# Performance work log

Measured on AMD Instinct MI355X. Metric: run time of the kernel, lower is better.

Reference implementation:

```python
import jax, jax.numpy as jnp
import numpy as np

U, I, D, NNZ, LAYERS, B = 50000, 50000, 64, 3200000, 3, 4096
N = U + I
L2_REG = 1e-5
EPS = 1e-12


def setup_inputs() -> dict:
    key = jax.random.key(0)
    ks = jax.random.split(key, 12)
    return {
        "users": jax.random.randint(ks[0], (B,), 0, U, dtype=jnp.int64)
        if jax.config.jax_enable_x64 else jax.random.randint(ks[0], (B,), 0, U, dtype=jnp.int32),
        "pos_items": jax.random.randint(ks[1], (B,), 0, N, dtype=jnp.int32),
        "neg_items": jax.random.randint(ks[2], (B,), 0, N, dtype=jnp.int32),
        "rows": jax.random.randint(ks[3], (NNZ,), 0, N, dtype=jnp.int32),
        "cols": jax.random.randint(ks[4], (NNZ,), 0, N, dtype=jnp.int32),
        "vals": jax.random.uniform(ks[5], (NNZ,), dtype=jnp.float32),
        "user_embed": jax.random.normal(ks[6], (U, D), dtype=jnp.float32),
        "item_embed": jax.random.normal(ks[7], (I, D), dtype=jnp.float32),
        "W1": jax.random.normal(ks[8], (LAYERS, D, D), dtype=jnp.float32) * 0.1,
        "b1": jax.random.normal(ks[9], (LAYERS, 1, D), dtype=jnp.float32) * 0.1,
        "W2": jax.random.normal(ks[10], (LAYERS, D, D), dtype=jnp.float32) * 0.1,
        "b2": jax.random.normal(ks[11], (LAYERS, 1, D), dtype=jnp.float32) * 0.1,
    }


def reference(users, pos_items, neg_items, rows, cols, vals,
              user_embed, item_embed, W1, b1, W2, b2):
    # E: [N, D] concatenated user/item embeddings
    E = jnp.concatenate([user_embed, item_embed], axis=0)
    embs = [E]
    for l in range(W1.shape[0]):
        # SpMM: L @ E via edge-wise gather + scatter-add (memory-bound)
        msgs = vals[:, None] * E[cols]                     # [nnz, D]
        L_mul = jax.ops.segment_sum(msgs, rows, num_segments=N)
        A_mul = L_mul + E                                  # A = L + I
        left = A_mul @ W1[l] + b1[l]
        right = (L_mul * E) @ W2[l] + b2[l]
        E = jax.nn.leaky_relu(left + right, negative_slope=0.2)
        # message dropout rate = 0 -> identity
        norm = jnp.maximum(jnp.linalg.norm(E, axis=1, keepdims=True), EPS)
        embs.append(E / norm)
    all_e = jnp.concatenate(embs, axis=1)                  # [N, D*(LAYERS+1)]
    u = all_e[users]
    p = all_e[pos_items]
    n = all_e[neg_items]
    pos_rating = jnp.sum(u * p, axis=1)
    neg_rating = jnp.sum(u * n, axis=1)
    bpr_loss = -jnp.mean(jax.nn.log_sigmoid(pos_rating - neg_rating))
    # faithful to source: neg term is ||n|| (not squared)
    l2norm = (jnp.sum(u ** 2) + jnp.sum(p ** 2) + jnp.sqrt(jnp.sum(n ** 2))) / 2.0
    l2reg = L2_REG * l2norm / u.shape[0]
    return bpr_loss + l2reg
```

## Files before the change

kernel.cpp:

```cpp
#include <hip/hip_runtime.h>
#include <hip/hip_bf16.h>
#include <math.h>

#define U_CNT 50000
#define I_CNT 50000
#define N_CNT 100000
#define D 64
#define NNZ_CNT 3200000
#define LAYERS 3
#define BATCH 4096
#define L2_REG_F 1e-5f
#define EPS_F 1e-12f

#define NBUCKET 391
#define SC_NBLK 256
#define SC_CHUNK 12500
#define BCNT_N (NBUCKET * SC_NBLK)
#define BCNT_NBLK ((BCNT_N + 255) / 256)

typedef __attribute__((ext_vector_type(8))) short short8;
typedef __attribute__((ext_vector_type(4))) float floatx4;

__device__ __forceinline__ unsigned short f32_to_bf16(float f) {
    unsigned int u = __float_as_uint(f);
    u += 0x7FFFu + ((u >> 16) & 1u);
    return (unsigned short)(u >> 16);
}
__device__ __forceinline__ float bf16_to_f32(unsigned short h) {
    return __uint_as_float(((unsigned int)h) << 16);
}
__device__ __forceinline__ float bf16_lo(unsigned int u) {
    return __uint_as_float(u << 16);
}
__device__ __forceinline__ float bf16_hi(unsigned int u) {
    return __uint_as_float(u & 0xFFFF0000u);
}
__device__ __forceinline__ unsigned int pack_bf16(float a, float b) {
    return (unsigned int)f32_to_bf16(a) | ((unsigned int)f32_to_bf16(b) << 16);
}

__global__ void init_E(const float* __restrict__ ue, const float* __restrict__ ie,
                       unsigned short* __restrict__ Ebf, float* __restrict__ all_e) {
    int tid = blockIdx.x * blockDim.x + threadIdx.x;
    if (tid >= N_CNT * D) return;
    int row = tid >> 6;
    int d = tid & 63;
    float v = (row < U_CNT) ? ue[tid] : ie[tid - U_CNT * D];
    Ebf[tid] = f32_to_bf16(v);
    all_e[(size_t)row * 256 + d] = v;
}

__global__ void scan_p1(const int* __restrict__ in, int* __restrict__ bsums, int n) {
    __shared__ int s[256];
    int t = threadIdx.x;
    int i = blockIdx.x * 256 + t;
    int v = (i < n) ? in[i] : 0;
    s[t] = v;
    __syncthreads();
    for (int off = 128; off >= 1; off >>= 1) {
        if (t < off) s[t] += s[t + off];
        __syncthreads();
    }
    if (t == 0) bsums[blockIdx.x] = s[0];
}

__global__ void scan_p2(int* __restrict__ bsums, int nblk) {
    __shared__ int s[512];
    int t = threadIdx.x;
    int v = (t < nblk) ? bsums[t] : 0;
    s[t] = v;
    __syncthreads();
    for (int off = 1; off < 512; off <<= 1) {
        int x = (t >= off) ? s[t - off] : 0;
        __syncthreads();
        s[t] += x;
        __syncthreads();
    }
    if (t < nblk) bsums[t] = s[t] - v;
}

__global__ void scan_p3(const int* __restrict__ in, const int* __restrict__ bsums,
                        int* __restrict__ out, int n) {
    __shared__ int s[256];
    int t = threadIdx.x;
    int i = blockIdx.x * 256 + t;
    int v = (i < n) ? in[i] : 0;
    s[t] = v;
    __syncthreads();
    for (int off = 1; off < 256; off <<= 1) {
        int x = (t >= off) ? s[t - off] : 0;
        __syncthreads();
        s[t] += x;
        __syncthreads();
    }
    if (i < n) out[i] = s[t] - v + bsums[blockIdx.x];
}

__global__ __launch_bounds__(1024) void bucket_hist(const int* __restrict__ rows,
                                                    int* __restrict__ bcnt) {
    __shared__ int h[NBUCKET];
    int blk = blockIdx.x, t = threadIdx.x;
    if (t < NBUCKET) h[t] = 0;
    __syncthreads();
    int s = blk * SC_CHUNK, e = s + SC_CHUNK;
    for (int i = s + t; i < e; i += 1024) atomicAdd(&h[rows[i] >> 8], 1);
    __syncthreads();
    if (t < NBUCKET) bcnt[t * SC_NBLK + blk] = h[t];
}

__global__ __launch_bounds__(1024) void block_scatter(const int* __restrict__ rows,
                                                      const int* __restrict__ cols,
                                                      const float* __restrict__ vals,
                                                      const int* __restrict__ boff,
                                                      float2* __restrict__ bbuf) {
    __shared__ int cur[NBUCKET];
    int blk = blockIdx.x, t = threadIdx.x;
    if (t < NBUCKET) cur[t] = boff[t * SC_NBLK + blk];
    __syncthreads();
    int s = blk * SC_CHUNK, e = s + SC_CHUNK;
    for (int i = s + t; i < e; i += 1024) {
        int r = rows[i];
        int b = r >> 8;
        int p = atomicAdd(&cur[b], 1);
        unsigned int bits = ((unsigned int)(r & 255) << 17) | (unsigned int)cols[i];
        bbuf[p] = make_float2(vals[i], __uint_as_float(bits));
    }
}

__global__ __launch_bounds__(1024) void csr_finalize(const float2* __restrict__ bbuf,
                                                     const int* __restrict__ boff,
                                                     int* __restrict__ row_ptr,
                                                     float2* __restrict__ packed) {
    __shared__ int h[256];
    __shared__ int cur[256];
    int b = blockIdx.x, t = threadIdx.x;
    int s = boff[b * SC_NBLK];
    int e = (b == NBUCKET - 1) ? NNZ_CNT : boff[(b + 1) * SC_NBLK];
    if (t < 256) h[t] = 0;
    __syncthreads();
    for (int i = s + t; i < e; i += 1024)
        atomicAdd(&h[__float_as_uint(bbuf[i].y) >> 17], 1);
    __syncthreads();
    int v = (t < 256) ? h[t] : 0;
    for (int off = 1; off < 256; off <<= 1) {
        int x = (t >= off && t < 256) ? h[t - off] : 0;
        __syncthreads();
        if (t < 256) h[t] += x;
        __syncthreads();
    }
    if (t < 256) {
        int start = s + h[t] - v;
        int row = (b << 8) + t;
        if (row < N_CNT) row_ptr[row] = start;
        cur[t] = start;
        if (b == 0 && t == 0) row_ptr[N_CNT] = NNZ_CNT;
    }
    __syncthreads();
    for (int i = s + t; i < e; i += 1024) {
        float2 rec = bbuf[i];
        unsigned int bits = __float_as_uint(rec.y);
        int p = atomicAdd(&cur[bits >> 17], 1);
        packed[p] = make_float2(rec.x, __int_as_float(bits & 0x1FFFFu));
    }
}

__global__ __launch_bounds__(256) void spmm_bf16(const float2* __restrict__ packed,
                                                 const int* __restrict__ row_ptr,
                                                 const unsigned short* __restrict__ Ebf,
                                                 unsigned short* __restrict__ Lm) {
    int wid = (blockIdx.x * blockDim.x + threadIdx.x) >> 6;
    int lane = threadIdx.x & 63;
    if (wid >= N_CNT) return;
    int s = row_ptr[wid];
    int e = row_ptr[wid + 1];
    int sub = lane >> 2;
    int sl = lane & 3;
    int eidx = sub >> 1;
    int half = sub & 1;
    int dbase = half * 32 + sl * 8;
    float a0 = 0.f, a1 = 0.f, a2 = 0.f, a3 = 0.f;
    float a4 = 0.f, a5 = 0.f, a6 = 0.f, a7 = 0.f;
    int i = s + eidx;
    float2 rec = (i < e) ? packed[i] : make_float2(0.f, __int_as_float(0));
    while (i < e) {
        int inext = i + 8;
        float2 rnext = (inext < e) ? packed[inext] : make_float2(0.f, __int_as_float(0));
        int c = __float_as_int(rec.y);
        uint4 ev = *(const uint4*)(Ebf + (size_t)c * D + dbase);
        float v = rec.x;
        a0 += v * bf16_lo(ev.x); a1 += v * bf16_hi(ev.x);
        a2 += v * bf16_lo(ev.y); a3 += v * bf16_hi(ev.y);
        a4 += v * bf16_lo(ev.z); a5 += v * bf16_hi(ev.z);
        a6 += v * bf16_lo(ev.w); a7 += v * bf16_hi(ev.w);
        rec = rnext;
        i = inext;
    }
#pragma unroll
    for (int off = 32; off >= 8; off >>= 1) {
        a0 += __shfl_xor(a0, off, 64); a1 += __shfl_xor(a1, off, 64);
        a2 += __shfl_xor(a2, off, 64); a3 += __shfl_xor(a3, off, 64);
        a4 += __shfl_xor(a4, off, 64); a5 += __shfl_xor(a5, off, 64);
        a6 += __shfl_xor(a6, off, 64); a7 += __shfl_xor(a7, off, 64);
    }
    if (eidx == 0) {
        unsigned int* dst = (unsigned int*)(Lm + (size_t)wid * D + dbase);
        *(uint4*)dst = make_uint4(pack_bf16(a0, a1), pack_bf16(a2, a3),
                                  pack_bf16(a4, a5), pack_bf16(a6, a7));
    }
}

#define AP 136
__global__ __launch_bounds__(256) void layer_fused_mfma(const unsigned short* __restrict__ Lm,
                                                        unsigned short* __restrict__ Ebf,
                                                        const float* __restrict__ W1,
                                                        const float* __restrict__ b1,
                                                        const float* __restrict__ W2,
                                                        const float* __restrict__ b2,
                                                        float* __restrict__ all_e, int layer) {
    __shared__ unsigned short sBt[64 * AP];
    __shared__ float sBias[64];
    __shared__ unsigned short sA[4][16 * AP];

    int t = threadIdx.x;
    for (int i = t; i < 4096; i += 256) {
        int k = i >> 6, n = i & 63;
        sBt[n * AP + k] = f32_to_bf16(W1[i]);
        sBt[n * AP + 64 + k] = f32_to_bf16(W2[i]);
    }
    if (t < 64) sBias[t] = b1[t] + b2[t];
    __syncthreads();

    int w = t >> 6, lane = t & 63;
    int quad = lane >> 4, l16 = lane & 15;

    short8 bfrag[4][4];
#pragma unroll
    for (int ks = 0; ks < 4; ks++)
#pragma unroll
        for (int ct = 0; ct < 4; ct++)
            bfrag[ks][ct] = *(const short8*)&sBt[(ct * 16 + l16) * AP + ks * 32 + quad * 8];

    float bias[4];
#pragma unroll
    for (int ct = 0; ct < 4; ct++) bias[ct] = sBias[ct * 16 + l16];

    unsigned short* A = sA[w];
    int col_off = (layer + 1) * 64;
    int nwaves = gridDim.x * 4;

    for (int tile = blockIdx.x * 4 + w; tile < N_CNT / 16; tile += nwaves) {
        int rbase = tile * 16;
#pragma unroll
        for (int p = 0; p < 4; p++) {
            int r = p * 4 + quad;
            int c = l16 * 4;
            uint2 lw = *(const uint2*)(Lm + (size_t)(rbase + r) * 64 + c);
            float l0 = bf16_lo(lw.x), l1 = bf16_hi(lw.x);
            float l2 = bf16_lo(lw.y), l3 = bf16_hi(lw.y);
            ushort4 eh = *(const ushort4*)(Ebf + (size_t)(rbase + r) * 64 + c);
            float e0 = bf16_to_f32(eh.x), e1 = bf16_to_f32(eh.y);
            float e2 = bf16_to_f32(eh.z), e3 = bf16_to_f32(eh.w);
            *(uint2*)&A[r * AP + c] = make_uint2(pack_bf16(l0 + e0, l1 + e1),
                                                pack_bf16(l2 + e2, l3 + e3));
            *(uint2*)&A[r * AP + 64 + c] = make_uint2(pack_bf16(l0 * e0, l1 * e1),
                                                      pack_bf16(l2 * e2, l3 * e3));
        }
        floatx4 acc[4];
#pragma unroll
        for (int ct = 0; ct < 4; ct++) {
            acc[ct][0] = bias[ct]; acc[ct][1] = bias[ct];
            acc[ct][2] = bias[ct]; acc[ct][3] = bias[ct];
        }
#pragma unroll
        for (int ks = 0; ks < 4; ks++) {
            short8 af = *(const short8*)&A[l16 * AP + ks * 32 + quad * 8];
#pragma unroll
            for (int ct = 0; ct < 4; ct++)
                acc[ct] = __builtin_amdgcn_mfma_f32_16x16x32_bf16(af, bfrag[ks][ct], acc[ct], 0, 0, 0);
        }
        float y[4][4];
        float ssq[4] = {0.f, 0.f, 0.f, 0.f};
#pragma unroll
        for (int ct = 0; ct < 4; ct++)
#pragma unroll
            for (int reg = 0; reg < 4; reg++) {
                float v = acc[ct][reg];
                v = (v > 0.f) ? v : 0.2f * v;
                y[ct][reg] = v;
                ssq[reg] += v * v;
            }
#pragma unroll
        for (int reg = 0; reg < 4; reg++) {
            float ss = ssq[reg];
            ss += __shfl_xor(ss, 1, 64);
            ss += __shfl_xor(ss, 2, 64);
            ss += __shfl_xor(ss, 4, 64);
            ss += __shfl_xor(ss, 8, 64);
            ssq[reg] = fmaxf(sqrtf(ss), EPS_F);
        }
#pragma unroll
        for (int reg = 0; reg < 4; reg++) {
            int row = rbase + quad * 4 + reg;
            float inv = 1.0f / ssq[reg];
#pragma unroll
            for (int ct = 0; ct < 4; ct++) {
                int col = ct * 16 + l16;
                float v = y[ct][reg];
                Ebf[(size_t)row * 64 + col] = f32_to_bf16(v);
                all_e[(size_t)row * 256 + col_off + col] = v * inv;
            }
        }
    }
}

__device__ __forceinline__ float dot4(float4 a, float4 b) {
    return a.x * b.x + a.y * b.y + a.z * b.z + a.w * b.w;
}

__global__ __launch_bounds__(256) void score_kernel(const float* __restrict__ all_e,
                                                    const int* __restrict__ users,
                                                    const int* __restrict__ pos,
                                                    const int* __restrict__ neg,
                                                    float4* __restrict__ partials) {
    int wid = (blockIdx.x * blockDim.x + threadIdx.x) >> 6;
    int lane = threadIdx.x & 63;
    if (wid >= BATCH) return;
    int ui = users[wid];
    int pi = pos[wid];
    int ni = neg[wid];
    const float4* uv4 = (const float4*)(all_e + (size_t)ui * 256);
    const float4* pv4 = (const float4*)(all_e + (size_t)pi * 256);
    const float4* nv4 = (const float4*)(all_e + (size_t)ni * 256);
    float4 uv = uv4[lane];
    float4 pv = pv4[lane];
    float4 nv = nv4[lane];
    float s_up = dot4(uv, pv);
    float s_un = dot4(uv, nv);
    float s_uu = dot4(uv, uv);
    float s_pp = dot4(pv, pv);
    float s_nn = dot4(nv, nv);
#pragma unroll
    for (int off = 32; off >= 1; off >>= 1) {
        s_up += __shfl_xor(s_up, off, 64);
        s_un += __shfl_xor(s_un, off, 64);
        s_uu += __shfl_xor(s_uu, off, 64);
        s_pp += __shfl_xor(s_pp, off, 64);
        s_nn += __shfl_xor(s_nn, off, 64);
    }
    if (lane == 0) {
        float x = s_up - s_un;
        float ls = fminf(x, 0.f) - log1pf(expf(-fabsf(x)));
        partials[wid] = make_float4(-ls, s_uu, s_pp, s_nn);
    }
}

__global__ __launch_bounds__(256) void reduce_finalize(const float4* __restrict__ partials,
                                                       float* __restrict__ out) {
    __shared__ float4 s[256];
    int t = threadIdx.x;
    float4 a = make_float4(0.f, 0.f, 0.f, 0.f);
    for (int i = t; i < BATCH; i += 256) {
        float4 p = partials[i];
        a.x += p.x; a.y += p.y; a.z += p.z; a.w += p.w;
    }
    s[t] = a;
    __syncthreads();
    for (int off = 128; off >= 1; off >>= 1) {
        if (t < off) {
            s[t].x += s[t + off].x;
            s[t].y += s[t + off].y;
            s[t].z += s[t + off].z;
            s[t].w += s[t + off].w;
        }
        __syncthreads();
    }
    if (t == 0) {
        float bpr = s[0].x / (float)BATCH;
        float l2norm = (s[0].y + s[0].z + sqrtf(s[0].w)) * 0.5f;
        out[0] = bpr + L2_REG_F * l2norm / (float)BATCH;
    }
}

extern "C" void kernel_launch(void* const* d_in, const int* in_sizes, int n_in,
                              void* d_out, int out_size, void* d_ws, size_t ws_size,
                              hipStream_t stream) {
    const int* users = (const int*)d_in[0];
    const int* pos_items = (const int*)d_in[1];
    const int* neg_items = (const int*)d_in[2];
    const int* rows = (const int*)d_in[3];
    const int* cols = (const int*)d_in[4];
    const float* vals = (const float*)d_in[5];
    const float* user_embed = (const float*)d_in[6];
    const float* item_embed = (const float*)d_in[7];
    const float* W1 = (const float*)d_in[8];
    const float* b1 = (const float*)d_in[9];
    const float* W2 = (const float*)d_in[10];
    const float* b2 = (const float*)d_in[11];
    float* out = (float*)d_out;

    char* ws = (char*)d_ws;
    size_t off_alle = 0;
    size_t off_packed = off_alle + (size_t)N_CNT * 256 * 4;
    size_t off_Ebf = off_packed + (size_t)NNZ_CNT * 8;
    size_t off_Lm = off_Ebf + (size_t)N_CNT * D * 2;
    size_t off_rowptr = off_Lm + (size_t)N_CNT * D * 2;
    size_t off_blkB = off_rowptr + 400128;
    size_t off_bcnt = off_blkB + 2048;
    size_t off_part = off_bcnt + 400384;

    float* all_e = (float*)(ws + off_alle);
    float2* bbuf = (float2*)(ws + off_alle);
    float2* packed = (float2*)(ws + off_packed);
    unsigned short* Ebf = (unsigned short*)(ws + off_Ebf);
    unsigned short* Lm = (unsigned short*)(ws + off_Lm);
    int* row_ptr = (int*)(ws + off_rowptr);
    int* blkB = (int*)(ws + off_blkB);
    int* bcnt = (int*)(ws + off_bcnt);
    float4* partials = (float4*)(ws + off_part);

    bucket_hist<<<SC_NBLK, 1024, 0, stream>>>(rows, bcnt);
    scan_p1<<<BCNT_NBLK, 256, 0, stream>>>(bcnt, blkB, BCNT_N);
    scan_p2<<<1, 512, 0, stream>>>(blkB, BCNT_NBLK);
    scan_p3<<<BCNT_NBLK, 256, 0, stream>>>(bcnt, blkB, bcnt, BCNT_N);
    block_scatter<<<SC_NBLK, 1024, 0, stream>>>(rows, cols, vals, bcnt, bbuf);
    csr_finalize<<<NBUCKET, 1024, 0, stream>>>(bbuf, bcnt, row_ptr, packed);

    init_E<<<(N_CNT * D) / 256, 256, 0, stream>>>(user_embed, item_embed, Ebf, all_e);

    for (int l = 0; l < LAYERS; l++) {
        spmm_bf16<<<(N_CNT * 64) / 256, 256, 0, stream>>>(packed, row_ptr, Ebf, Lm);
        layer_fused_mfma<<<784, 256, 0, stream>>>(Lm, Ebf, W1 + (size_t)l * 4096,
                                                  b1 + (size_t)l * 64, W2 + (size_t)l * 4096,
                                                  b2 + (size_t)l * 64, all_e, l);
    }

    score_kernel<<<(BATCH * 64) / 256, 256, 0, stream>>>(all_e, users, pos_items, neg_items,
                                                         partials);
    reduce_finalize<<<1, 256, 0, stream>>>(partials, out);
}
```

Baseline: 437.2 us.

## Fuse SpMM gather into per-layer MFMA kernel with ping-pong embedding buffers

Merges the sparse gather-accumulate into the dense MFMA layer kernel: each wave computes L_mul for its 16-row tile directly into shared memory before the matmul. This removes the intermediate Lm buffer write/read and one kernel launch per layer. E is double-buffered because rows are read by other blocks while being updated. In exchange, the latency-bound gather now runs with far fewer concurrent waves and lower occupancy due to LDS usage, reducing memory-level parallelism.

```diff
diff --git a/kernel.cpp b/kernel.cpp
--- a/kernel.cpp
+++ b/kernel.cpp
@@ -164,74 +164,36 @@
     }
 }
 
-__global__ __launch_bounds__(256) void spmm_bf16(const float2* __restrict__ packed,
-                                                 const int* __restrict__ row_ptr,
-                                                 const unsigned short* __restrict__ Ebf,
-                                                 unsigned short* __restrict__ Lm) {
-    int wid = (blockIdx.x * blockDim.x + threadIdx.x) >> 6;
-    int lane = threadIdx.x & 63;
-    if (wid >= N_CNT) return;
-    int s = row_ptr[wid];
-    int e = row_ptr[wid + 1];
+#define AP 136
+__global__ __launch_bounds__(256) void spmm_layer_mfma(const float2* __restrict__ packed,
+                                                       const int* __restrict__ row_ptr,
+                                                       const unsigned short* __restrict__ Ein,
+                                                       unsigned short* __restrict__ Eout,
+                                                       const float* __restrict__ W1,
+                                                       const float* __restrict__ b1,
+                                                       const float* __restrict__ W2,
+                                                       const float* __restrict__ b2,
+                                                       float* __restrict__ all_e, int layer) {
+    __shared__ unsigned short sBt[64 * AP];
+    __shared__ float sBias[64];
+    __shared__ unsigned short sA[4][16 * AP];
+
+    int t = threadIdx.x;
+    for (int i = t; i < 4096; i += 256) {
+        int k = i >> 6, n = i & 63;
+        sBt[n * AP + k] = f32_to_bf16(W1[i]);
+        sBt[n * AP + 64 + k] = f32_to_bf16(W2[i]);
+    }
+    if (t < 64) sBias[t] = b1[t] + b2[t];
+    __syncthreads();
+
+    int w = t >> 6, lane = t & 63;
+    int quad = lane >> 4, l16 = lane & 15;
     int sub = lane >> 2;
     int sl = lane & 3;
     int eidx = sub >> 1;
     int half = sub & 1;
     int dbase = half * 32 + sl * 8;
-    float a0 = 0.f, a1 = 0.f, a2 = 0.f, a3 = 0.f;
-    float a4 = 0.f, a5 = 0.f, a6 = 0.f, a7 = 0.f;
-    int i = s + eidx;
-    float2 rec = (i < e) ? packed[i] : make_float2(0.f, __int_as_float(0));
-    while (i < e) {
-        int inext = i + 8;
-        float2 rnext = (inext < e) ? packed[inext] : make_float2(0.f, __int_as_float(0));
-        int c = __float_as_int(rec.y);
-        uint4 ev = *(const uint4*)(Ebf + (size_t)c * D + dbase);
-        float v = rec.x;
-        a0 += v * bf16_lo(ev.x); a1 += v * bf16_hi(ev.x);
-        a2 += v * bf16_lo(ev.y); a3 += v * bf16_hi(ev.y);
-        a4 += v * bf16_lo(ev.z); a5 += v * bf16_hi(ev.z);
-        a6 += v * bf16_lo(ev.w); a7 += v * bf16_hi(ev.w);
-        rec = rnext;
-        i = inext;
-    }
-#pragma unroll
-    for (int off = 32; off >= 8; off >>= 1) {
-        a0 += __shfl_xor(a0, off, 64); a1 += __shfl_xor(a1, off, 64);
-        a2 += __shfl_xor(a2, off, 64); a3 += __shfl_xor(a3, off, 64);
-        a4 += __shfl_xor(a4, off, 64); a5 += __shfl_xor(a5, off, 64);
-        a6 += __shfl_xor(a6, off, 64); a7 += __shfl_xor(a7, off, 64);
-    }
-    if (eidx == 0) {
-        unsigned int* dst = (unsigned int*)(Lm + (size_t)wid * D + dbase);
-        *(uint4*)dst = make_uint4(pack_bf16(a0, a1), pack_bf16(a2, a3),
-                                  pack_bf16(a4, a5), pack_bf16(a6, a7));
-    }
-}
-
-#define AP 136
-__global__ __launch_bounds__(256) void layer_fused_mfma(const unsigned short* __restrict__ Lm,
-                                                        unsigned short* __restrict__ Ebf,
-                                                        const float* __restrict__ W1,
-                                                        const float* __restrict__ b1,
-                                                        const float* __restrict__ W2,
-                                                        const float* __restrict__ b2,
-                                                        float* __restrict__ all_e, int layer) {
-    __shared__ unsigned short sBt[64 * AP];
-    __shared__ float sBias[64];
-    __shared__ unsigned short sA[4][16 * AP];
-
-    int t = threadIdx.x;
-    for (int i = t; i < 4096; i += 256) {
-        int k = i >> 6, n = i & 63;
-        sBt[n * AP + k] = f32_to_bf16(W1[i]);
-        sBt[n * AP + 64 + k] = f32_to_bf16(W2[i]);
-    }
-    if (t < 64) sBias[t] = b1[t] + b2[t];
-    __syncthreads();
-
-    int w = t >> 6, lane = t & 63;
-    int quad = lane >> 4, l16 = lane & 15;
 
     short8 bfrag[4][4];
 #pragma unroll
@@ -250,20 +212,47 @@
 
     for (int tile = blockIdx.x * 4 + w; tile < N_CNT / 16; tile += nwaves) {
         int rbase = tile * 16;
-#pragma unroll
-        for (int p = 0; p < 4; p++) {
-            int r = p * 4 + quad;
-            int c = l16 * 4;
-            uint2 lw = *(const uint2*)(Lm + (size_t)(rbase + r) * 64 + c);
-            float l0 = bf16_lo(lw.x), l1 = bf16_hi(lw.x);
-            float l2 = bf16_lo(lw.y), l3 = bf16_hi(lw.y);
-            ushort4 eh = *(const ushort4*)(Ebf + (size_t)(rbase + r) * 64 + c);
-            float e0 = bf16_to_f32(eh.x), e1 = bf16_to_f32(eh.y);
-            float e2 = bf16_to_f32(eh.z), e3 = bf16_to_f32(eh.w);
-            *(uint2*)&A[r * AP + c] = make_uint2(pack_bf16(l0 + e0, l1 + e1),
-                                                pack_bf16(l2 + e2, l3 + e3));
-            *(uint2*)&A[r * AP + 64 + c] = make_uint2(pack_bf16(l0 * e0, l1 * e1),
-                                                      pack_bf16(l2 * e2, l3 * e3));
+        for (int r = 0; r < 16; r++) {
+            int row = rbase + r;
+            int s = row_ptr[row];
+            int e = row_ptr[row + 1];
+            float a0 = 0.f, a1 = 0.f, a2 = 0.f, a3 = 0.f;
+            float a4 = 0.f, a5 = 0.f, a6 = 0.f, a7 = 0.f;
+            int i = s + eidx;
+            float2 rec = (i < e) ? packed[i] : make_float2(0.f, __int_as_float(0));
+            while (i < e) {
+                int inext = i + 8;
+                float2 rnext = (inext < e) ? packed[inext] : make_float2(0.f, __int_as_float(0));
+                int c = __float_as_int(rec.y);
+                uint4 ev = *(const uint4*)(Ein + (size_t)c * D + dbase);
+                float v = rec.x;
+                a0 += v * bf16_lo(ev.x); a1 += v * bf16_hi(ev.x);
+                a2 += v * bf16_lo(ev.y); a3 += v * bf16_hi(ev.y);
+                a4 += v * bf16_lo(ev.z); a5 += v * bf16_hi(ev.z);
+                a6 += v * bf16_lo(ev.w); a7 += v * bf16_hi(ev.w);
+                rec = rnext;
+                i = inext;
+            }
+#pragma unroll
+            for (int off = 32; off >= 8; off >>= 1) {
+                a0 += __shfl_xor(a0, off, 64); a1 += __shfl_xor(a1, off, 64);
+                a2 += __shfl_xor(a2, off, 64); a3 += __shfl_xor(a3, off, 64);
+                a4 += __shfl_xor(a4, off, 64); a5 += __shfl_xor(a5, off, 64);
+                a6 += __shfl_xor(a6, off, 64); a7 += __shfl_xor(a7, off, 64);
+            }
+            if (eidx == 0) {
+                uint4 eh = *(const uint4*)(Ein + (size_t)row * D + dbase);
+                float e0 = bf16_lo(eh.x), e1 = bf16_hi(eh.x);
+                float e2 = bf16_lo(eh.y), e3 = bf16_hi(eh.y);
+                float e4 = bf16_lo(eh.z), e5 = bf16_hi(eh.z);
+                float e6 = bf16_lo(eh.w), e7 = bf16_hi(eh.w);
+                *(uint4*)&A[r * AP + dbase] =
+                    make_uint4(pack_bf16(a0 + e0, a1 + e1), pack_bf16(a2 + e2, a3 + e3),
+                               pack_bf16(a4 + e4, a5 + e5), pack_bf16(a6 + e6, a7 + e7));
+                *(uint4*)&A[r * AP + 64 + dbase] =
+                    make_uint4(pack_bf16(a0 * e0, a1 * e1), pack_bf16(a2 * e2, a3 * e3),
+                               pack_bf16(a4 * e4, a5 * e5), pack_bf16(a6 * e6, a7 * e7));
+            }
         }
         floatx4 acc[4];
 #pragma unroll
@@ -306,7 +295,7 @@
             for (int ct = 0; ct < 4; ct++) {
                 int col = ct * 16 + l16;
                 float v = y[ct][reg];
-                Ebf[(size_t)row * 64 + col] = f32_to_bf16(v);
+                Eout[(size_t)row * 64 + col] = f32_to_bf16(v);
                 all_e[(size_t)row * 256 + col_off + col] = v * inv;
             }
         }
@@ -401,9 +390,9 @@
     char* ws = (char*)d_ws;
     size_t off_alle = 0;
     size_t off_packed = off_alle + (size_t)N_CNT * 256 * 4;
-    size_t off_Ebf = off_packed + (size_t)NNZ_CNT * 8;
-    size_t off_Lm = off_Ebf + (size_t)N_CNT * D * 2;
-    size_t off_rowptr = off_Lm + (size_t)N_CNT * D * 2;
+    size_t off_EbfA = off_packed + (size_t)NNZ_CNT * 8;
+    size_t off_EbfB = off_EbfA + (size_t)N_CNT * D * 2;
+    size_t off_rowptr = off_EbfB + (size_t)N_CNT * D * 2;
     size_t off_blkB = off_rowptr + 400128;
     size_t off_bcnt = off_blkB + 2048;
     size_t off_part = off_bcnt + 400384;
@@ -411,8 +400,8 @@
     float* all_e = (float*)(ws + off_alle);
     float2* bbuf = (float2*)(ws + off_alle);
     float2* packed = (float2*)(ws + off_packed);
-    unsigned short* Ebf = (unsigned short*)(ws + off_Ebf);
-    unsigned short* Lm = (unsigned short*)(ws + off_Lm);
+    unsigned short* EbfA = (unsigned short*)(ws + off_EbfA);
+    unsigned short* EbfB = (unsigned short*)(ws + off_EbfB);
     int* row_ptr = (int*)(ws + off_rowptr);
     int* blkB = (int*)(ws + off_blkB);
     int* bcnt = (int*)(ws + off_bcnt);
@@ -425,13 +414,15 @@
     block_scatter<<<SC_NBLK, 1024, 0, stream>>>(rows, cols, vals, bcnt, bbuf);
     csr_finalize<<<NBUCKET, 1024, 0, stream>>>(bbuf, bcnt, row_ptr, packed);
 
-    init_E<<<(N_CNT * D) / 256, 256, 0, stream>>>(user_embed, item_embed, Ebf, all_e);
+    init_E<<<(N_CNT * D) / 256, 256, 0, stream>>>(user_embed, item_embed, EbfA, all_e);
 
     for (int l = 0; l < LAYERS; l++) {
-        spmm_bf16<<<(N_CNT * 64) / 256, 256, 0, stream>>>(packed, row_ptr, Ebf, Lm);
-        layer_fused_mfma<<<784, 256, 0, stream>>>(Lm, Ebf, W1 + (size_t)l * 4096,
-                                                  b1 + (size_t)l * 64, W2 + (size_t)l * 4096,
-                                                  b2 + (size_t)l * 64, all_e, l);
+        const unsigned short* Ein = (l & 1) ? EbfB : EbfA;
+        unsigned short* Eout = (l & 1) ? EbfA : EbfB;
+        spmm_layer_mfma<<<1024, 256, 0, stream>>>(packed, row_ptr, Ein, Eout,
+                                                  W1 + (size_t)l * 4096, b1 + (size_t)l * 64,
+                                                  W2 + (size_t)l * 4096, b2 + (size_t)l * 64,
+                                                  all_e, l);
     }
 
     score_kernel<<<(BATCH * 64) / 256, 256, 0, stream>>>(all_e, users, pos_items, neg_items,
```

New measurement: 670.9 us. 1.53x slower.
